# Kernel optimization log

Hardware: AMD Instinct MI355X
Metric: run time of the kernel (lower is better)

The kernel has to match this reference:

```python
import jax, jax.numpy as jnp
import numpy as np

B, N, E = 4, 8192, 131072
NODE_F, EDGE_F, HID, ACT = 16, 1, 128, 8


def _glorot(key, shape):
    fan_in, fan_out = shape[0], shape[1]
    lim = np.sqrt(6.0 / (fan_in + fan_out))
    return jax.random.uniform(key, shape, jnp.float32, -lim, lim)


def setup_inputs() -> dict:
    key = jax.random.key(0)
    ks = jax.random.split(key, 20)
    inp = {
        'node_features': jax.random.randint(ks[0], (B, N, NODE_F), 0, 10, jnp.int32),
        'edge_index': jax.random.randint(ks[1], (B, 2, E), 0, N, jnp.int64),
        'edge_features': jax.random.normal(ks[2], (B, E, EDGE_F), jnp.float32),
        # conv1: in = 2*NODE_F + EDGE_F
        'c1_w1': _glorot(ks[3], (2 * NODE_F + EDGE_F, HID)), 'c1_b1': jnp.zeros((HID,), jnp.float32),
        'c1_w2': _glorot(ks[4], (HID, HID)), 'c1_b2': jnp.zeros((HID,), jnp.float32),
        # conv2/conv3: in = 2*HID + 1
        'c2_w1': _glorot(ks[5], (2 * HID + 1, HID)), 'c2_b1': jnp.zeros((HID,), jnp.float32),
        'c2_w2': _glorot(ks[6], (HID, HID)), 'c2_b2': jnp.zeros((HID,), jnp.float32),
        'c3_w1': _glorot(ks[7], (2 * HID + 1, HID)), 'c3_b1': jnp.zeros((HID,), jnp.float32),
        'c3_w2': _glorot(ks[8], (HID, HID)), 'c3_b2': jnp.zeros((HID,), jnp.float32),
        'lin_w': _glorot(ks[9], (NODE_F + HID, ACT)), 'lin_b': jnp.zeros((ACT,), jnp.float32),
    }
    return inp


def _edge_conv(x, src, dst, ea, w1, b1, w2, b2):
    # message: cat([x_i (target), x_j (source), edge_attr]) -> Linear -> LeakyReLU -> Linear
    m = jnp.concatenate([x[dst], x[src], ea], axis=1)          # [E, 2F+EF]
    m = jax.nn.leaky_relu(m @ w1 + b1) @ w2 + b2               # [E, out]
    out = jax.ops.segment_min(m, dst, num_segments=x.shape[0])  # min-aggregate at targets
    cnt = jnp.zeros((x.shape[0],), m.dtype).at[dst].add(1.0)
    return jnp.where(cnt[:, None] > 0, out, 0.0)                # nodes w/o in-edges -> 0 (PyG)


def _graph_fwd(x0, ei, ea, p):
    x0 = x0.astype(jnp.float32)  # torch casts to IntTensor then MLP promotes; math on integer values
    src, dst = ei[0], ei[1]      # flow='source_to_target'
    x = jax.nn.leaky_relu(_edge_conv(x0, src, dst, ea, p['c1_w1'], p['c1_b1'], p['c1_w2'], p['c1_b2']))
    x = jax.nn.leaky_relu(_edge_conv(x, src, dst, ea, p['c2_w1'], p['c2_b1'], p['c2_w2'], p['c2_b2']))
    x = jax.nn.leaky_relu(_edge_conv(x, src, dst, ea, p['c3_w1'], p['c3_b1'], p['c3_w2'], p['c3_b2']))
    x = jnp.concatenate([x0, x], axis=1)
    return jax.nn.softplus(x @ p['lin_w'] + p['lin_b'])         # [N, ACT]


def reference(node_features, edge_index, edge_features,
              c1_w1, c1_b1, c1_w2, c1_b2,
              c2_w1, c2_b1, c2_w2, c2_b2,
              c3_w1, c3_b1, c3_w2, c3_b2,
              lin_w, lin_b):
    p = dict(c1_w1=c1_w1, c1_b1=c1_b1, c1_w2=c1_w2, c1_b2=c1_b2,
             c2_w1=c2_w1, c2_b1=c2_b1, c2_w2=c2_w2, c2_b2=c2_b2,
             c3_w1=c3_w1, c3_b1=c3_b1, c3_w2=c3_w2, c3_b2=c3_b2,
             lin_w=lin_w, lin_b=lin_b)
    return jax.vmap(lambda x, ei, ea: _graph_fwd(x, ei, ea, p))(
        node_features, edge_index, edge_features)               # [B, N, ACT]
```

## Files before the change

### kernel.cpp

```cpp
#include <hip/hip_runtime.h>

#define B_ 4
#define N_ 8192
#define E_ 131072
#define HID_ 128

typedef unsigned short us8 __attribute__((ext_vector_type(8)));
typedef unsigned short us4 __attribute__((ext_vector_type(4)));
typedef unsigned int   ui4 __attribute__((ext_vector_type(4)));
typedef int            i4  __attribute__((ext_vector_type(4)));
typedef __bf16         v8bf __attribute__((ext_vector_type(8)));
typedef float          v4f  __attribute__((ext_vector_type(4)));
typedef float          v2f  __attribute__((ext_vector_type(2)));

#define KEY_INF 0xFF800000u

__device__ __forceinline__ float b2f(unsigned short u) {
    return __uint_as_float(((unsigned)u) << 16);
}
__device__ __forceinline__ unsigned short f2b(float f) {
    unsigned x = __float_as_uint(f);
    return (unsigned short)((x + 0x7fffu + ((x >> 16) & 1u)) >> 16);
}
__device__ __forceinline__ unsigned fkey(float f) {
    unsigned b = __float_as_uint(f);
    return (b & 0x80000000u) ? ~b : (b | 0x80000000u);
}
__device__ __forceinline__ float funkey(unsigned k) {
    unsigned b = (k & 0x80000000u) ? (k ^ 0x80000000u) : ~k;
    return __uint_as_float(b);
}

__device__ __forceinline__ void repack_one(const float* __restrict__ w1, const float* __restrict__ w2,
                                           unsigned short* __restrict__ w1n, unsigned short* __restrict__ w2t,
                                           int F, int KPAD, int gid) {
    int t1 = 256 * KPAD;
    if (gid < t1) {
        int j = gid / KPAD, k = gid - j * KPAD;
        float v = 0.f;
        if (k < F) v = (j < 128) ? w1[k * 128 + j] : w1[(F + k) * 128 + (j - 128)];
        w1n[gid] = f2b(v);
    } else {
        int g = gid - t1;
        if (g < 16384) { int j = g >> 7, k = g & 127; w2t[g] = f2b(w2[k * 128 + j]); }
    }
}

__global__ void k_setup(const int* __restrict__ nf, unsigned short* __restrict__ x0b,
                        unsigned* __restrict__ cnt, unsigned* __restrict__ agg,
                        const float* __restrict__ w1a, const float* __restrict__ w2a,
                        const float* __restrict__ w1b, const float* __restrict__ w2b,
                        const float* __restrict__ w1c, const float* __restrict__ w2c,
                        unsigned short* __restrict__ w1n0, unsigned short* __restrict__ w2t0,
                        unsigned short* __restrict__ w1n1, unsigned short* __restrict__ w2t1,
                        unsigned short* __restrict__ w1n2, unsigned short* __restrict__ w2t2) {
    const int bid = blockIdx.x, tid = threadIdx.x;
    if (bid >= 4096) {
        const int rb = bid - 4096;
        const int gid = rb * 256 + tid;
        if (rb < 96)       repack_one(w1a, w2a, w1n0, w2t0, 16, 32, gid);
        else if (rb < 288) repack_one(w1b, w2b, w1n1, w2t1, 128, 128, gid - 96 * 256);
        else               repack_one(w1c, w2c, w1n2, w2t2, 128, 128, gid - 288 * 256);
        return;
    }
    const int gid = bid * 256 + tid;
    ui4 v = {KEY_INF, KEY_INF, KEY_INF, KEY_INF};
    ((ui4*)agg)[gid] = v;
    if (bid < 512) {
        i4 x = ((const i4*)nf)[gid];
        us4 o;
        o[0] = f2b((float)x[0]); o[1] = f2b((float)x[1]);
        o[2] = f2b((float)x[2]); o[3] = f2b((float)x[3]);
        ((us4*)x0b)[gid] = o;
    }
    if (bid < 128) cnt[gid] = 0u;
}

__global__ void k_hist(const int* __restrict__ ei, unsigned* __restrict__ cnt) {
    int gid = blockIdx.x * 256 + threadIdx.x;
    int b = gid >> 17, e = gid & (E_ - 1);
    int dst = ei[(b << 18) + E_ + e];
    atomicAdd(&cnt[(b << 13) + dst], 1u);
}

__global__ __launch_bounds__(1024) void k_scan(unsigned* __restrict__ cnt) {
    int b = blockIdx.x;
    __shared__ unsigned ps[1024];
    unsigned* c = cnt + (b << 13) + threadIdx.x * 8;
    unsigned loc[8]; unsigned s = 0;
#pragma unroll
    for (int i = 0; i < 8; i++) { loc[i] = c[i]; s += loc[i]; }
    ps[threadIdx.x] = s;
    __syncthreads();
    for (int off = 1; off < 1024; off <<= 1) {
        unsigned v = (threadIdx.x >= (unsigned)off) ? ps[threadIdx.x - off] : 0u;
        __syncthreads();
        ps[threadIdx.x] += v;
        __syncthreads();
    }
    unsigned run = ps[threadIdx.x] - s;
#pragma unroll
    for (int i = 0; i < 8; i++) { c[i] = run; run += loc[i]; }
}

__global__ void k_scatter(const int* __restrict__ ei, unsigned* __restrict__ wptr,
                          int* __restrict__ perm) {
    int gid = blockIdx.x * 256 + threadIdx.x;
    int b = gid >> 17, e = gid & (E_ - 1);
    int dst = ei[(b << 18) + E_ + e];
    unsigned pos = atomicAdd(&wptr[(b << 13) + dst], 1u);
    perm[(b << 17) + pos] = e;
}

template<int KPAD, bool FROM_AGG>
__global__ __launch_bounds__(256, 3) void k_node(
    const unsigned short* __restrict__ xin,
    unsigned* __restrict__ agg,
    const unsigned short* __restrict__ w1n,
    const float* __restrict__ bias1,
    unsigned short* __restrict__ Yd,
    unsigned short* __restrict__ Ys)
{
    constexpr int ASTR = KPAD + 8;
    __shared__ __align__(16) unsigned short A[64 * ASTR];
    __shared__ __align__(16) unsigned short Yb[64 * 264];

    const int tid = threadIdx.x;
    const int wave = tid >> 6, lane = tid & 63, lq = lane >> 4, lm = lane & 15;
    const int tile = (blockIdx.x & 7) * 64 + (blockIdx.x >> 3);
    const int n0 = tile * 64;

    v8bf wf[4][KPAD / 32]; float b1v[4];
#pragma unroll
    for (int nt = 0; nt < 4; nt++) {
        const int col = wave * 64 + nt * 16 + lm;
#pragma unroll
        for (int ks = 0; ks < KPAD / 32; ks++)
            wf[nt][ks] = *(const v8bf*)&w1n[col * KPAD + ks * 32 + lq * 8];
        b1v[nt] = (col < 128) ? bias1[col] : 0.f;
    }

    {
        const int row = tid >> 2, p = tid & 3;
        if (FROM_AGG) {
#pragma unroll
            for (int i = 0; i < 8; i++) {
                const int c = p + 4 * i;
                unsigned* ap = agg + ((size_t)(n0 + row)) * 128 + c * 4;
                ui4 k = *(ui4*)ap;
                ui4 inf = {KEY_INF, KEY_INF, KEY_INF, KEY_INF};
                *(ui4*)ap = inf;
                us4 o;
#pragma unroll
                for (int j = 0; j < 4; j++) {
                    float v = (k[j] == KEY_INF) ? 0.f : funkey(k[j]);
                    v = (v > 0.f) ? v : 0.01f * v;
                    o[j] = f2b(v);
                }
                *(us4*)&A[row * ASTR + c * 4] = o;
            }
        } else {
            us4 v = *(const us4*)(xin + ((size_t)(n0 + row)) * 16 + p * 4);
            *(us4*)&A[row * ASTR + p * 4] = v;
            us4 z = {0, 0, 0, 0};
            *(us4*)&A[row * ASTR + 16 + p * 4] = z;
        }
    }
    __syncthreads();

#pragma unroll
    for (int mt = 0; mt < 4; mt++) {
        v4f acc[4];
#pragma unroll
        for (int nt = 0; nt < 4; nt++) acc[nt] = v4f{0.f, 0.f, 0.f, 0.f};
#pragma unroll
        for (int ks = 0; ks < KPAD / 32; ks++) {
            v8bf a = *(const v8bf*)&A[(mt * 16 + lm) * ASTR + ks * 32 + lq * 8];
#pragma unroll
            for (int nt = 0; nt < 4; nt++)
                acc[nt] = __builtin_amdgcn_mfma_f32_16x16x32_bf16(a, wf[nt][ks], acc[nt], 0, 0, 0);
        }
#pragma unroll
        for (int nt = 0; nt < 4; nt++) {
            const int col = wave * 64 + nt * 16 + lm;
#pragma unroll
            for (int r = 0; r < 4; r++)
                Yb[(mt * 16 + lq * 4 + r) * 264 + col] = f2b(acc[nt][r] + b1v[nt]);
        }
    }
    __syncthreads();

    const int bb = tile >> 7, nl0 = (tile & 127) * 64;
#pragma unroll
    for (int i = 0; i < 8; i++) {
        const int idx = tid + 256 * i;
        const int row = idx >> 5, c = idx & 31;
        us8 v = *(const us8*)&Yb[row * 264 + c * 8];
        const int col0 = c * 8;
        unsigned short* dp = (col0 < 128)
            ? (Yd + ((size_t)(bb * N_) + nl0 + row) * 128 + col0)
            : (Ys + ((size_t)(bb * N_) + nl0 + row) * 128 + (col0 - 128));
        *(us8*)dp = v;
    }
}

__global__ __launch_bounds__(256, 4) void k_edge(
    const unsigned short* __restrict__ Yd,
    const unsigned short* __restrict__ Ys,
    const int* __restrict__ ei,
    const float* __restrict__ eaf,
    const int* __restrict__ perm,
    const unsigned short* __restrict__ w2t,
    const float* __restrict__ weap,
    const float* __restrict__ bias2,
    unsigned* __restrict__ agg)
{
    __shared__ __align__(16) unsigned short Hs[128 * 128];
    __shared__ __align__(16) int   dstl[128];
    __shared__ __align__(16) float weal[128];

    const int tid = threadIdx.x;
    const int wave = tid >> 6, lane = tid & 63, lq = lane >> 4, lm = lane & 15;

    if (tid < 128) weal[tid] = weap[tid];

    v8bf w2f[2][4]; float b2v[2];
#pragma unroll
    for (int nt = 0; nt < 2; nt++) {
        const int col = wave * 32 + nt * 16 + lm;
#pragma unroll
        for (int ks = 0; ks < 4; ks++)
            w2f[nt][ks] = *(const v8bf*)&w2t[col * 128 + ks * 32 + lq * 8];
        b2v[nt] = bias2[col];
    }
    __syncthreads();

    const int arow = tid >> 1, p = tid & 1;
    const int s = ((arow & 0x70) >> 2) | ((arow & 0x0C) << 3) | (arow & 3);
    const int rsw = arow & 15;

    int t = (blockIdx.x & 7) * 512 + (blockIdx.x >> 3);
    int b = t >> 10;
    int e = perm[(b << 17) + (t & 1023) * 128 + s];
    int src = ei[(b << 18) + e];
    int dst = ei[(b << 18) + E_ + e];
    float ea = eaf[(b << 17) + e];
    const ui4* ydp = (const ui4*)(Yd + ((size_t)(b * N_) + dst) * 128);
    const ui4* ysp = (const ui4*)(Ys + ((size_t)(b * N_) + src) * 128);
    ui4 va0 = ydp[p], vb0 = ysp[p];

    for (int jj = 0; jj < 4; jj++) {
        const int curb = b;
        if (p == 0) dstl[s] = dst;

        {
            const v2f eav2 = {ea, ea};
            const v2f c01  = {0.01f, 0.01f};
            ui4 va = va0, vb = vb0;
#pragma unroll
            for (int i = 0; i < 8; i++) {
                ui4 na, nb;
                if (i < 7) { na = ydp[p + 2 * (i + 1)]; nb = ysp[p + 2 * (i + 1)]; }
                const int c = p + 2 * i;
                ui4 od;
#pragma unroll
                for (int k = 0; k < 4; k++) {
                    v2f a, bb2, z;
                    a[0]   = __uint_as_float(va[k] << 16);
                    a[1]   = __uint_as_float(va[k] & 0xffff0000u);
                    bb2[0] = __uint_as_float(vb[k] << 16);
                    bb2[1] = __uint_as_float(vb[k] & 0xffff0000u);
                    v2f wv = *(const v2f*)&weal[c * 8 + 2 * k];
                    z = a + bb2 + wv * eav2;
                    z = __builtin_elementwise_max(z, z * c01);
                    od[k] = __builtin_amdgcn_perm(__float_as_uint(z[1]) + 0x8000u,
                                                  __float_as_uint(z[0]) + 0x8000u,
                                                  0x07060302u);
                }
                *(ui4*)&Hs[arow * 128 + ((c ^ rsw) * 8)] = od;
                va = na; vb = nb;
            }
        }
        __syncthreads();

        t += 128;
        if (jj < 3) {
            b = t >> 10;
            e = perm[(b << 17) + (t & 1023) * 128 + s];
            src = ei[(b << 18) + e];
            dst = ei[(b << 18) + E_ + e];
            ea = eaf[(b << 17) + e];
            ydp = (const ui4*)(Yd + ((size_t)(b * N_) + dst) * 128);
            ysp = (const ui4*)(Ys + ((size_t)(b * N_) + src) * 128);
            va0 = ydp[p]; vb0 = ysp[p];
        }

        {
            const int col0 = wave * 32 + lm, col1 = col0 + 16;
            unsigned* aggb = agg + (size_t)(curb * N_) * 128;
            float cur0 = 0.f, cur1 = 0.f; int curd = -1;
#pragma unroll
            for (int mt = 0; mt < 8; mt++) {
                const int row = mt * 16 + lm;
                v4f acc0 = {b2v[0], b2v[0], b2v[0], b2v[0]};
                v4f acc1 = {b2v[1], b2v[1], b2v[1], b2v[1]};
#pragma unroll
                for (int ks = 0; ks < 4; ks++) {
                    v8bf a = *(const v8bf*)&Hs[row * 128 + (((ks * 4 + lq) ^ lm) * 8)];
                    acc0 = __builtin_amdgcn_mfma_f32_16x16x32_bf16(a, w2f[0][ks], acc0, 0, 0, 0);
                    acc1 = __builtin_amdgcn_mfma_f32_16x16x32_bf16(a, w2f[1][ks], acc1, 0, 0, 0);
                }
                i4 dv = *(const i4*)&dstl[lq * 32 + mt * 4];
#pragma unroll
                for (int r = 0; r < 4; r++) {
                    const float v0 = acc0[r];
                    const float v1 = acc1[r];
                    const int d = dv[r];
                    if (d != curd) {
                        if (curd >= 0) {
                            atomicMin(aggb + (size_t)curd * 128 + col0, fkey(cur0));
                            atomicMin(aggb + (size_t)curd * 128 + col1, fkey(cur1));
                        }
                        curd = d; cur0 = v0; cur1 = v1;
                    } else {
                        cur0 = fminf(cur0, v0); cur1 = fminf(cur1, v1);
                    }
                }
            }
            atomicMin(aggb + (size_t)curd * 128 + col0, fkey(cur0));
            atomicMin(aggb + (size_t)curd * 128 + col1, fkey(cur1));
        }
        __syncthreads();
    }
}

__global__ __launch_bounds__(256, 4) void k_final(
    const unsigned short* __restrict__ x0b, const unsigned* __restrict__ agg,
    const float* __restrict__ lw, const float* __restrict__ lb,
    float* __restrict__ out) {
    __shared__ float w[144 * 8];
    __shared__ float bias8[8];
    __shared__ float xs[64 * 129];
    const int tid = threadIdx.x;
    for (int i = tid; i < 1152; i += 256) w[i] = lw[i];
    if (tid < 8) bias8[tid] = lb[tid];
    const int n0 = blockIdx.x * 64;
#pragma unroll
    for (int i = 0; i < 8; i++) {
        const int idx = tid + 256 * i;
        const int row = idx >> 5, c = idx & 31;
        ui4 k = ((const ui4*)(agg + ((size_t)(n0 + row)) * 128))[c];
#pragma unroll
        for (int j = 0; j < 4; j++) {
            float v = (k[j] == KEY_INF) ? 0.f : funkey(k[j]);
            v = fmaxf(v, 0.01f * v);
            xs[row * 129 + c * 4 + j] = v;
        }
    }
    __syncthreads();
    const int node = tid >> 2, ap = (tid & 3) * 2;
    float a0 = bias8[ap], a1 = bias8[ap + 1];
    const unsigned short* x0 = x0b + (size_t)(n0 + node) * 16;
#pragma unroll
    for (int f = 0; f < 16; f++) {
        const float xv = b2f(x0[f]);
        a0 += xv * w[f * 8 + ap]; a1 += xv * w[f * 8 + ap + 1];
    }
    const float* xr = &xs[node * 129];
#pragma unroll 8
    for (int f = 0; f < 128; f++) {
        const float xv = xr[f];
        a0 += xv * w[(16 + f) * 8 + ap]; a1 += xv * w[(16 + f) * 8 + ap + 1];
    }
    v2f o;
    o[0] = fmaxf(a0, 0.f) + log1pf(expf(-fabsf(a0)));
    o[1] = fmaxf(a1, 0.f) + log1pf(expf(-fabsf(a1)));
    *(v2f*)&out[(size_t)(n0 + node) * 8 + ap] = o;
}

extern "C" void kernel_launch(void* const* d_in, const int* in_sizes, int n_in,
                              void* d_out, int out_size, void* d_ws, size_t ws_size,
                              hipStream_t stream) {
    (void)in_sizes; (void)n_in; (void)out_size; (void)ws_size;
    const int* nf  = (const int*)d_in[0];
    const int* ei  = (const int*)d_in[1];
    const float* eaf = (const float*)d_in[2];
    const float* cw1[3] = {(const float*)d_in[3],  (const float*)d_in[7],  (const float*)d_in[11]};
    const float* cb1[3] = {(const float*)d_in[4],  (const float*)d_in[8],  (const float*)d_in[12]};
    const float* cw2[3] = {(const float*)d_in[5],  (const float*)d_in[9],  (const float*)d_in[13]};
    const float* cb2[3] = {(const float*)d_in[6],  (const float*)d_in[10], (const float*)d_in[14]};
    const float* lw = (const float*)d_in[15];
    const float* lb = (const float*)d_in[16];
    float* out = (float*)d_out;

    size_t off = 0;
    auto carve = [&](size_t bytes) { void* p = (char*)d_ws + off; off += (bytes + 255) & ~(size_t)255; return p; };
    unsigned short* x0b  = (unsigned short*)carve((size_t)B_ * N_ * 16 * 2);
    unsigned*       agg  = (unsigned*)carve((size_t)B_ * N_ * 128 * 4);
    unsigned*       cnt  = (unsigned*)carve((size_t)B_ * N_ * 4);
    int*            perm = (int*)carve((size_t)B_ * E_ * 4);
    unsigned short* Yd   = (unsigned short*)carve((size_t)B_ * N_ * 128 * 2);
    unsigned short* Ys   = (unsigned short*)carve((size_t)B_ * N_ * 128 * 2);
    unsigned short* w1n0 = (unsigned short*)carve(256 * 32 * 2);
    unsigned short* w2t0 = (unsigned short*)carve(128 * 128 * 2);
    unsigned short* w1n1 = (unsigned short*)carve(256 * 128 * 2);
    unsigned short* w2t1 = (unsigned short*)carve(128 * 128 * 2);
    unsigned short* w1n2 = (unsigned short*)carve(256 * 128 * 2);
    unsigned short* w2t2 = (unsigned short*)carve(128 * 128 * 2);

    k_setup<<<4576, 256, 0, stream>>>(nf, x0b, cnt, agg,
                                      cw1[0], cw2[0], cw1[1], cw2[1], cw1[2], cw2[2],
                                      w1n0, w2t0, w1n1, w2t1, w1n2, w2t2);
    k_hist<<<2048, 256, 0, stream>>>(ei, cnt);
    k_scan<<<B_, 1024, 0, stream>>>(cnt);
    k_scatter<<<2048, 256, 0, stream>>>(ei, cnt, perm);

    k_node<32, false><<<512, 256, 0, stream>>>(x0b, agg, w1n0, cb1[0], Yd, Ys);
    k_edge<<<1024, 256, 0, stream>>>(Yd, Ys, ei, eaf, perm, w2t0, cw1[0] + 32 * 128, cb2[0], agg);

    k_node<128, true><<<512, 256, 0, stream>>>(x0b, agg, w1n1, cb1[1], Yd, Ys);
    k_edge<<<1024, 256, 0, stream>>>(Yd, Ys, ei, eaf, perm, w2t1, cw1[1] + 256 * 128, cb2[1], agg);

    k_node<128, true><<<512, 256, 0, stream>>>(x0b, agg, w1n2, cb1[2], Yd, Ys);
    k_edge<<<1024, 256, 0, stream>>>(Yd, Ys, ei, eaf, perm, w2t2, cw1[2] + 256 * 128, cb2[2], agg);

    k_final<<<512, 256, 0, stream>>>(x0b, agg, lw, lb, out);
}
```

Before: 316.5 us.

## Double-buffer edge tiles in LDS with 64-edge tiles to overlap gather and MFMA

The edge kernel now works on 64-edge tiles instead of 128 and keeps two LDS buffers for the hidden activations and destination indices. While one buffer feeds the MFMA and atomic-min aggregation, the gather and LeakyReLU for the next tile write into the other, so only one barrier per iteration is needed. Each thread now handles a quarter of a row instead of half. This aims to hide gather latency behind compute and cut one sync per tile. In exchange, the smaller tiles mean more loop iterations, shorter runs of equal destinations (so more atomics), and a different permutation mapping.

```diff
diff --git a/kernel.cpp b/kernel.cpp
--- a/kernel.cpp
+++ b/kernel.cpp
@@ -215,8 +215,8 @@
     const float* __restrict__ bias2,
     unsigned* __restrict__ agg)
 {
-    __shared__ __align__(16) unsigned short Hs[128 * 128];
-    __shared__ __align__(16) int   dstl[128];
+    __shared__ __align__(16) unsigned short Hs[2][64 * 128];
+    __shared__ __align__(16) int   dstl[2][64];
     __shared__ __align__(16) float weal[128];
 
     const int tid = threadIdx.x;
@@ -233,66 +233,61 @@
             w2f[nt][ks] = *(const v8bf*)&w2t[col * 128 + ks * 32 + lq * 8];
         b2v[nt] = bias2[col];
     }
-    __syncthreads();
-
-    const int arow = tid >> 1, p = tid & 1;
-    const int s = ((arow & 0x70) >> 2) | ((arow & 0x0C) << 3) | (arow & 3);
+
+    const int arow = tid >> 2, p = tid & 3;
+    const int s = ((arow & 0x0C) << 2) | ((arow >> 2) & 0x0C) | (arow & 3);
     const int rsw = arow & 15;
 
-    int t = (blockIdx.x & 7) * 512 + (blockIdx.x >> 3);
-    int b = t >> 10;
-    int e = perm[(b << 17) + (t & 1023) * 128 + s];
+    int t = (blockIdx.x & 7) * 1024 + (blockIdx.x >> 3);
+    int b = t >> 11;
+    int e = perm[(b << 17) + (t & 2047) * 64 + s];
     int src = ei[(b << 18) + e];
     int dst = ei[(b << 18) + E_ + e];
     float ea = eaf[(b << 17) + e];
-    const ui4* ydp = (const ui4*)(Yd + ((size_t)(b * N_) + dst) * 128);
-    const ui4* ysp = (const ui4*)(Ys + ((size_t)(b * N_) + src) * 128);
-    ui4 va0 = ydp[p], vb0 = ysp[p];
-
-    for (int jj = 0; jj < 4; jj++) {
-        const int curb = b;
-        if (p == 0) dstl[s] = dst;
-
-        {
-            const v2f eav2 = {ea, ea};
-            const v2f c01  = {0.01f, 0.01f};
-            ui4 va = va0, vb = vb0;
-#pragma unroll
-            for (int i = 0; i < 8; i++) {
-                ui4 na, nb;
-                if (i < 7) { na = ydp[p + 2 * (i + 1)]; nb = ysp[p + 2 * (i + 1)]; }
-                const int c = p + 2 * i;
-                ui4 od;
-#pragma unroll
-                for (int k = 0; k < 4; k++) {
-                    v2f a, bb2, z;
-                    a[0]   = __uint_as_float(va[k] << 16);
-                    a[1]   = __uint_as_float(va[k] & 0xffff0000u);
-                    bb2[0] = __uint_as_float(vb[k] << 16);
-                    bb2[1] = __uint_as_float(vb[k] & 0xffff0000u);
-                    v2f wv = *(const v2f*)&weal[c * 8 + 2 * k];
-                    z = a + bb2 + wv * eav2;
-                    z = __builtin_elementwise_max(z, z * c01);
-                    od[k] = __builtin_amdgcn_perm(__float_as_uint(z[1]) + 0x8000u,
-                                                  __float_as_uint(z[0]) + 0x8000u,
-                                                  0x07060302u);
-                }
-                *(ui4*)&Hs[arow * 128 + ((c ^ rsw) * 8)] = od;
-                va = na; vb = nb;
+
+    {
+        const ui4* ydp = (const ui4*)(Yd + ((size_t)(b * N_) + dst) * 128);
+        const ui4* ysp = (const ui4*)(Ys + ((size_t)(b * N_) + src) * 128);
+        if (p == 0) dstl[0][s] = dst;
+        const v2f eav2 = {ea, ea};
+        const v2f c01  = {0.01f, 0.01f};
+        ui4 va = ydp[p], vb = ysp[p];
+#pragma unroll
+        for (int i = 0; i < 4; i++) {
+            ui4 na, nb;
+            if (i < 3) { na = ydp[p + 4 * (i + 1)]; nb = ysp[p + 4 * (i + 1)]; }
+            const int c = p + 4 * i;
+            ui4 od;
+#pragma unroll
+            for (int k = 0; k < 4; k++) {
+                v2f a, bb2, z;
+                a[0]   = __uint_as_float(va[k] << 16);
+                a[1]   = __uint_as_float(va[k] & 0xffff0000u);
+                bb2[0] = __uint_as_float(vb[k] << 16);
+                bb2[1] = __uint_as_float(vb[k] & 0xffff0000u);
+                v2f wv = *(const v2f*)&weal[c * 8 + 2 * k];
+                z = a + bb2 + wv * eav2;
+                z = __builtin_elementwise_max(z, z * c01);
+                od[k] = __builtin_amdgcn_perm(__float_as_uint(z[1]) + 0x8000u,
+                                              __float_as_uint(z[0]) + 0x8000u,
+                                              0x07060302u);
             }
-        }
-        __syncthreads();
+            *(ui4*)&Hs[0][arow * 128 + ((c ^ rsw) * 8)] = od;
+            va = na; vb = nb;
+        }
+    }
+    __syncthreads();
+
+    for (int jj = 0; jj < 8; jj++) {
+        const int curb = b, buf = jj & 1;
 
         t += 128;
-        if (jj < 3) {
-            b = t >> 10;
-            e = perm[(b << 17) + (t & 1023) * 128 + s];
+        if (jj < 7) {
+            b = t >> 11;
+            e = perm[(b << 17) + (t & 2047) * 64 + s];
             src = ei[(b << 18) + e];
             dst = ei[(b << 18) + E_ + e];
             ea = eaf[(b << 17) + e];
-            ydp = (const ui4*)(Yd + ((size_t)(b * N_) + dst) * 128);
-            ysp = (const ui4*)(Ys + ((size_t)(b * N_) + src) * 128);
-            va0 = ydp[p]; vb0 = ysp[p];
         }
 
         {
@@ -300,17 +295,17 @@
             unsigned* aggb = agg + (size_t)(curb * N_) * 128;
             float cur0 = 0.f, cur1 = 0.f; int curd = -1;
 #pragma unroll
-            for (int mt = 0; mt < 8; mt++) {
+            for (int mt = 0; mt < 4; mt++) {
                 const int row = mt * 16 + lm;
                 v4f acc0 = {b2v[0], b2v[0], b2v[0], b2v[0]};
                 v4f acc1 = {b2v[1], b2v[1], b2v[1], b2v[1]};
 #pragma unroll
                 for (int ks = 0; ks < 4; ks++) {
-                    v8bf a = *(const v8bf*)&Hs[row * 128 + (((ks * 4 + lq) ^ lm) * 8)];
+                    v8bf a = *(const v8bf*)&Hs[buf][row * 128 + (((ks * 4 + lq) ^ lm) * 8)];
                     acc0 = __builtin_amdgcn_mfma_f32_16x16x32_bf16(a, w2f[0][ks], acc0, 0, 0, 0);
                     acc1 = __builtin_amdgcn_mfma_f32_16x16x32_bf16(a, w2f[1][ks], acc1, 0, 0, 0);
                 }
-                i4 dv = *(const i4*)&dstl[lq * 32 + mt * 4];
+                i4 dv = *(const i4*)&dstl[buf][lq * 16 + mt * 4];
 #pragma unroll
                 for (int r = 0; r < 4; r++) {
                     const float v0 = acc0[r];
@@ -330,6 +325,38 @@
             atomicMin(aggb + (size_t)curd * 128 + col0, fkey(cur0));
             atomicMin(aggb + (size_t)curd * 128 + col1, fkey(cur1));
         }
+
+        if (jj < 7) {
+            const ui4* ydp = (const ui4*)(Yd + ((size_t)(b * N_) + dst) * 128);
+            const ui4* ysp = (const ui4*)(Ys + ((size_t)(b * N_) + src) * 128);
+            if (p == 0) dstl[buf ^ 1][s] = dst;
+            const v2f eav2 = {ea, ea};
+            const v2f c01  = {0.01f, 0.01f};
+            ui4 va = ydp[p], vb = ysp[p];
+#pragma unroll
+            for (int i = 0; i < 4; i++) {
+                ui4 na, nb;
+                if (i < 3) { na = ydp[p + 4 * (i + 1)]; nb = ysp[p + 4 * (i + 1)]; }
+                const int c = p + 4 * i;
+                ui4 od;
+#pragma unroll
+                for (int k = 0; k < 4; k++) {
+                    v2f a, bb2, z;
+                    a[0]   = __uint_as_float(va[k] << 16);
+                    a[1]   = __uint_as_float(va[k] & 0xffff0000u);
+                    bb2[0] = __uint_as_float(vb[k] << 16);
+                    bb2[1] = __uint_as_float(vb[k] & 0xffff0000u);
+                    v2f wv = *(const v2f*)&weal[c * 8 + 2 * k];
+                    z = a + bb2 + wv * eav2;
+                    z = __builtin_elementwise_max(z, z * c01);
+                    od[k] = __builtin_amdgcn_perm(__float_as_uint(z[1]) + 0x8000u,
+                                                  __float_as_uint(z[0]) + 0x8000u,
+                                                  0x07060302u);
+                }
+                *(ui4*)&Hs[buf ^ 1][arow * 128 + ((c ^ rsw) * 8)] = od;
+                va = na; vb = nb;
+            }
+        }
         __syncthreads();
     }
 }
```

Measured after the change: 306.2 us. 1.03x faster.
